# Optimization experiments

Measured on AMD Instinct MI355X. Metric: run time of the kernel, lower is better.

## Reference

```python
import jax, jax.numpy as jnp
import numpy as np

B, N, C = 8, 1024, 768
H, D = 12, 64  # num_heads, head_dim
SCALE = D ** -0.5


def setup_inputs() -> dict:
    key = jax.random.key(0)
    ks = jax.random.split(key, 6)
    x = jax.random.normal(ks[0], (B, N, C), dtype=jnp.float32)
    # per-head Linear weights stacked: [H, D, C] (torch Linear stores [out, in])
    Wq = jax.random.normal(ks[1], (H, D, C), dtype=jnp.float32) * 0.02
    Wk = jax.random.normal(ks[2], (H, D, C), dtype=jnp.float32) * 0.02
    Wv = jax.random.normal(ks[3], (H, D, C), dtype=jnp.float32) * 0.02
    Wp = jax.random.normal(ks[4], (C, C), dtype=jnp.float32) * 0.02
    bp = jnp.zeros((C,), dtype=jnp.float32)
    return {"x": x, "Wq": Wq, "Wk": Wk, "Wv": Wv, "Wp": Wp, "bp": bp}


def reference(x, Wq, Wk, Wv, Wp, bp):
    # Per-head projections (batched across heads): [B, H, N, D]
    q = jnp.einsum('bnc,hdc->bhnd', x, Wq) * SCALE
    k = jnp.einsum('bnc,hdc->bhnd', x, Wk)
    v = jnp.einsum('bnc,hdc->bhnd', x, Wv)
    # Scaled dot-product attention per head
    attn = jax.nn.softmax(jnp.einsum('bhnd,bhmd->bhnm', q, k), axis=-1)
    out = jnp.einsum('bhnm,bhmd->bhnd', attn, v)
    # Concat heads along last dim == transpose to [B, N, H, D] then reshape
    out = out.transpose(0, 2, 1, 3).reshape(x.shape[0], x.shape[1], -1)
    # Output projection
    return out @ Wp.T + bp
```

## Files before the change

### kernel.cpp

```cpp
#include <hip/hip_runtime.h>

typedef unsigned short u16;
typedef __attribute__((ext_vector_type(8))) __bf16 bf16x8;
typedef __attribute__((ext_vector_type(4))) float f32x4;
typedef __attribute__((ext_vector_type(16))) float f32x16;

__device__ __forceinline__ u16 f2bf(float f) {
    union { float f; unsigned u; } v; v.f = f;
    unsigned u = v.u;
    u += 0x7FFFu + ((u >> 16) & 1u);
    return (u16)(u >> 16);
}

__device__ __forceinline__ unsigned pk2(float lo, float hi) {
    union { __bf16 h[2]; unsigned u; } x;
    x.h[0] = (__bf16)lo; x.h[1] = (__bf16)hi;
    return x.u;
}
__device__ __forceinline__ void pswap(unsigned &a, unsigned &b) {
    auto r = __builtin_amdgcn_permlane32_swap(a, b, false, false);
    a = r[0]; b = r[1];
}

typedef const __attribute__((address_space(1))) void GV;
typedef __attribute__((address_space(3))) void LV;
__device__ __forceinline__ void gl2lds16(const void* g, void* l) {
    __builtin_amdgcn_global_load_lds((GV*)g, (LV*)l, 16, 0, 0);
}

__global__ __launch_bounds__(256) void cast_all(
    const float* __restrict__ x,  const float* __restrict__ Wq,
    const float* __restrict__ Wk, const float* __restrict__ Wv,
    const float* __restrict__ Wp,
    u16* __restrict__ xb, u16* __restrict__ wb, u16* __restrict__ wpb)
{
    int bid = blockIdx.x;
    const float4* s; ushort4* d; int idx;
    if (bid < 6144) {
        s = (const float4*)x; d = (ushort4*)xb; idx = bid * 256 + threadIdx.x;
    } else {
        int t = bid - 6144;
        int w = t / 576;
        idx = (t - w * 576) * 256 + threadIdx.x;
        s = (const float4*)(w == 0 ? Wq : w == 1 ? Wk : w == 2 ? Wv : Wp);
        d = (ushort4*)(w == 3 ? wpb : wb + w * 589824);
    }
    float4 f = s[idx];
    ushort4 o;
    o.x = f2bf(f.x); o.y = f2bf(f.y); o.z = f2bf(f.z); o.w = f2bf(f.w);
    d[idx] = o;
}

__device__ __forceinline__ void stage_c(const u16* src, int k0, u16* lds, int i) {
    int line = i >> 3, pos = i & 7;
    int p = pos ^ (line & 7);
    int r = line * 2 + (p >> 2), c = p & 3;
    gl2lds16(src + (size_t)r * 768 + k0 + c * 8, lds + i * 8);
}
__device__ __forceinline__ const bf16x8* fragK(const u16* lds, int row, int quad) {
    int line = row >> 1;
    int pos = (((row & 1) << 2) | quad) ^ (line & 7);
    return reinterpret_cast<const bf16x8*>(lds + line * 64 + pos * 8);
}

__global__ __launch_bounds__(512, 4) void gemm_qkv(
    const u16* __restrict__ A, const u16* __restrict__ Bm,
    u16* __restrict__ qo, u16* __restrict__ ko, u16* __restrict__ vto)
{
    __shared__ u16 As[3][8192];
    __shared__ u16 Bs[3][4096];
    const int tid = threadIdx.x;
    const int wave = tid >> 6, lane = tid & 63;
    const int quad = lane >> 4, l16 = lane & 15;
    const int wm = wave >> 1, wn = wave & 1;
    const int id = blockIdx.x + 18 * blockIdx.y;
    const int nid = (id & 7) * 72 + (id >> 3);
    const int bx = nid % 18, by = nid / 18;
    const int rowBase = by * 256;
    const int colBase = bx * 128;

    const u16* aSrc = A + (size_t)rowBase * 768;
    const u16* bSrc = Bm + (size_t)colBase * 768;
    f32x4 acc[4][4] = {};

    #pragma unroll
    for (int tt = 0; tt < 2; tt++) {
        stage_c(aSrc, tt * 32, As[tt], tid);
        stage_c(aSrc, tt * 32, As[tt], 512 + tid);
        stage_c(bSrc, tt * 32, Bs[tt], tid);
    }
    asm volatile("s_waitcnt vmcnt(3)" ::: "memory");
    __builtin_amdgcn_s_barrier();
    asm volatile("" ::: "memory");

    int buf = 0;
    for (int t = 0; t < 24; t++) {
        bf16x8 a[4], b[4];
        #pragma unroll
        for (int mi = 0; mi < 4; mi++) a[mi] = *fragK(As[buf], wm * 64 + mi * 16 + l16, quad);
        #pragma unroll
        for (int ni = 0; ni < 4; ni++) b[ni] = *fragK(Bs[buf], wn * 64 + ni * 16 + l16, quad);
        int sb = buf + 2; if (sb >= 3) sb -= 3;
        if (t + 2 < 24) {
            int k2 = (t + 2) * 32;
            stage_c(aSrc, k2, As[sb], tid);
            stage_c(aSrc, k2, As[sb], 512 + tid);
            stage_c(bSrc, k2, Bs[sb], tid);
        }
        if (t <= 21)      asm volatile("s_waitcnt vmcnt(3)" ::: "memory");
        else if (t == 22) asm volatile("s_waitcnt vmcnt(0)" ::: "memory");
        __builtin_amdgcn_s_barrier();
        asm volatile("" ::: "memory");
        __builtin_amdgcn_s_setprio(1);
        #pragma unroll
        for (int mi = 0; mi < 4; mi++)
            #pragma unroll
            for (int ni = 0; ni < 4; ni++)
                acc[mi][ni] = __builtin_amdgcn_mfma_f32_16x16x32_bf16(a[mi], b[ni], acc[mi][ni], 0, 0, 0);
        __builtin_amdgcn_s_setprio(0);
        buf = (buf == 2) ? 0 : buf + 1;
    }

    #pragma unroll
    for (int mi = 0; mi < 4; mi++) {
        #pragma unroll
        for (int ni = 0; ni < 4; ni++) {
            int gj = colBase + wn * 64 + ni * 16 + l16;
            int which = gj / 768;
            int r = gj - which * 768;
            int h = r >> 6, d = r & 63;
            int gi0 = rowBase + wm * 64 + mi * 16 + quad * 4;
            int b_ = gi0 >> 10;
            int n0 = gi0 & 1023;
            if (which == 2) {
                ushort4 pk;
                pk.x = f2bf(acc[mi][ni][0]);
                pk.y = f2bf(acc[mi][ni][1]);
                pk.z = f2bf(acc[mi][ni][2]);
                pk.w = f2bf(acc[mi][ni][3]);
                *reinterpret_cast<ushort4*>(vto + ((size_t)(b_ * 12 + h) * 64 + d) * 1024 + n0) = pk;
            } else {
                float s = (which == 0) ? 0.125f : 1.0f;
                u16* dst = (which == 0 ? qo : ko) + ((size_t)(b_ * 12 + h) * 1024 + n0) * 64 + d;
                #pragma unroll
                for (int rr = 0; rr < 4; rr++)
                    dst[(size_t)rr * 64] = f2bf(acc[mi][ni][rr] * s);
            }
        }
    }
}

__global__ __launch_bounds__(256, 3) void attn_fwd(
    const u16* __restrict__ q, const u16* __restrict__ k,
    const u16* __restrict__ vt, u16* __restrict__ ao)
{
    __shared__ u16 Ks[2][4096];
    __shared__ u16 Vs[2][4096];
    const int bh = blockIdx.x, qt = blockIdx.y;
    const int b = bh / 12, h = bh - b * 12;
    const int tid = threadIdx.x;
    const int wave = tid >> 6, lane = tid & 63;
    const int l31 = lane & 31, hi = lane >> 5;
    const int sw = l31 & 7;

    const u16* qb = q + (size_t)bh * 65536 + ((size_t)qt * 128 + wave * 32) * 64;
    const u16* kb = k + (size_t)bh * 65536;
    const u16* vb = vt + (size_t)bh * 65536;

    auto stage = [&](int buf, int j0) {
        #pragma unroll
        for (int r = 0; r < 2; r++) {
            int i = r * 256 + tid;
            int row = i >> 3, cp = i & 7;
            int cl = cp ^ (row & 7);
            gl2lds16((const char*)kb + (size_t)(j0 + row) * 128 + cl * 16,
                     (char*)&Ks[buf][0] + i * 16);
        }
        #pragma unroll
        for (int r = 0; r < 2; r++) {
            int i = r * 256 + tid;
            int row = i >> 3, cp = i & 7;
            int cl = cp ^ (row & 7);
            gl2lds16((const char*)vb + (size_t)row * 2048 + (size_t)j0 * 2 + cl * 16,
                     (char*)&Vs[buf][0] + i * 16);
        }
    };

    stage(0, 0);

    bf16x8 qf[4];
    #pragma unroll
    for (int dk = 0; dk < 4; dk++)
        qf[dk] = *reinterpret_cast<const bf16x8*>(qb + l31 * 64 + dk * 16 + hi * 8);

    f32x16 o0 = {}, o1 = {};
    float lsum = 0.f;

    __syncthreads();

    int buf = 0;
    for (int j0 = 0; j0 < 1024; j0 += 64) {
        if (j0 + 64 < 1024) stage(buf ^ 1, j0 + 64);

        f32x16 s0 = {}, s1 = {};
        #pragma unroll
        for (int dk = 0; dk < 4; dk++) {
            int ch = ((2 * dk + hi) ^ sw) * 8;
            bf16x8 kf0 = *reinterpret_cast<const bf16x8*>(&Ks[buf][l31 * 64 + ch]);
            bf16x8 kf1 = *reinterpret_cast<const bf16x8*>(&Ks[buf][(32 + l31) * 64 + ch]);
            s0 = __builtin_amdgcn_mfma_f32_32x32x16_bf16(kf0, qf[dk], s0, 0, 0, 0);
            s1 = __builtin_amdgcn_mfma_f32_32x32x16_bf16(kf1, qf[dk], s1, 0, 0, 0);
        }

        bf16x8 pa[4];
        #pragma unroll
        for (int kbk = 0; kbk < 2; kbk++) {
            float p[16];
            #pragma unroll
            for (int r = 0; r < 16; r++) {
                p[r] = __expf(kbk ? s1[r] : s0[r]);
                lsum += p[r];
            }
            unsigned W00 = pk2(p[0],  p[1]),  W01 = pk2(p[2],  p[3]);
            unsigned W10 = pk2(p[4],  p[5]),  W11 = pk2(p[6],  p[7]);
            unsigned W20 = pk2(p[8],  p[9]),  W21 = pk2(p[10], p[11]);
            unsigned W30 = pk2(p[12], p[13]), W31 = pk2(p[14], p[15]);
            pswap(W00, W10); pswap(W01, W11);
            pswap(W20, W30); pswap(W21, W31);
            union { unsigned u[4]; bf16x8 v; } pk0, pk1;
            pk0.u[0] = W00; pk0.u[1] = W01; pk0.u[2] = W10; pk0.u[3] = W11;
            pk1.u[0] = W20; pk1.u[1] = W21; pk1.u[2] = W30; pk1.u[3] = W31;
            pa[kbk * 2 + 0] = pk0.v;
            pa[kbk * 2 + 1] = pk1.v;
        }

        #pragma unroll
        for (int ks = 0; ks < 4; ks++) {
            int ch = ((2 * ks + hi) ^ sw) * 8;
            bf16x8 vf0 = *reinterpret_cast<const bf16x8*>(&Vs[buf][l31 * 64 + ch]);
            bf16x8 vf1 = *reinterpret_cast<const bf16x8*>(&Vs[buf][(32 + l31) * 64 + ch]);
            o0 = __builtin_amdgcn_mfma_f32_32x32x16_bf16(pa[ks], vf0, o0, 0, 0, 0);
            o1 = __builtin_amdgcn_mfma_f32_32x32x16_bf16(pa[ks], vf1, o1, 0, 0, 0);
        }

        __syncthreads();
        buf ^= 1;
    }

    lsum += __shfl_xor(lsum, 32, 64);

    #pragma unroll
    for (int r = 0; r < 16; r++) {
        int qrow = (r & 3) + 8 * (r >> 2) + 4 * hi;
        float lv = __shfl(lsum, qrow, 32);
        float inv = 1.0f / lv;
        int n = qt * 128 + wave * 32 + qrow;
        size_t base = (size_t)(b * 1024 + n) * 768 + h * 64;
        ao[base + l31]      = f2bf(o0[r] * inv);
        ao[base + 32 + l31] = f2bf(o1[r] * inv);
    }
}

__global__ __launch_bounds__(256, 3) void gemm_proj(
    const u16* __restrict__ A, const u16* __restrict__ Bm,
    const float* __restrict__ bias, float* __restrict__ out)
{
    __shared__ u16 As[3][4096];
    __shared__ u16 Bs[3][4096];
    const int tid = threadIdx.x;
    const int wave = tid >> 6, lane = tid & 63;
    const int quad = lane >> 4, l16 = lane & 15;
    const int wr = (wave >> 1) * 64, wc = (wave & 1) * 64;
    const int id = blockIdx.x + 6 * blockIdx.y;
    const int nid = (id & 7) * 48 + (id >> 3);
    const int bx = nid % 6, by = nid / 6;
    const int rowBase = by * 128;
    const int colBase = bx * 128;

    const u16* aSrc = A + (size_t)rowBase * 768;
    const u16* bSrc = Bm + (size_t)colBase * 768;
    f32x4 acc[4][4] = {};

    #pragma unroll
    for (int tt = 0; tt < 2; tt++) {
        stage_c(aSrc, tt * 32, As[tt], tid);
        stage_c(aSrc, tt * 32, As[tt], 256 + tid);
        stage_c(bSrc, tt * 32, Bs[tt], tid);
        stage_c(bSrc, tt * 32, Bs[tt], 256 + tid);
    }
    asm volatile("s_waitcnt vmcnt(4)" ::: "memory");
    __builtin_amdgcn_s_barrier();
    asm volatile("" ::: "memory");

    int buf = 0;
    for (int t = 0; t < 24; t++) {
        bf16x8 a[4], b[4];
        #pragma unroll
        for (int mi = 0; mi < 4; mi++) a[mi] = *fragK(As[buf], wr + mi * 16 + l16, quad);
        #pragma unroll
        for (int ni = 0; ni < 4; ni++) b[ni] = *fragK(Bs[buf], wc + ni * 16 + l16, quad);
        int sb = buf + 2; if (sb >= 3) sb -= 3;
        if (t + 2 < 24) {
            int k2 = (t + 2) * 32;
            stage_c(aSrc, k2, As[sb], tid);
            stage_c(aSrc, k2, As[sb], 256 + tid);
            stage_c(bSrc, k2, Bs[sb], tid);
            stage_c(bSrc, k2, Bs[sb], 256 + tid);
        }
        if (t <= 21)      asm volatile("s_waitcnt vmcnt(4)" ::: "memory");
        else if (t == 22) asm volatile("s_waitcnt vmcnt(0)" ::: "memory");
        __builtin_amdgcn_s_barrier();
        asm volatile("" ::: "memory");
        __builtin_amdgcn_s_setprio(1);
        #pragma unroll
        for (int mi = 0; mi < 4; mi++)
            #pragma unroll
            for (int ni = 0; ni < 4; ni++)
                acc[mi][ni] = __builtin_amdgcn_mfma_f32_16x16x32_bf16(a[mi], b[ni], acc[mi][ni], 0, 0, 0);
        __builtin_amdgcn_s_setprio(0);
        buf = (buf == 2) ? 0 : buf + 1;
    }

    #pragma unroll
    for (int mi = 0; mi < 4; mi++) {
        #pragma unroll
        for (int ni = 0; ni < 4; ni++) {
            int gj = colBase + wc + ni * 16 + l16;
            float bv = bias[gj];
            int gi0 = rowBase + wr + mi * 16 + quad * 4;
            #pragma unroll
            for (int rr2 = 0; rr2 < 4; rr2++)
                out[(size_t)(gi0 + rr2) * 768 + gj] = acc[mi][ni][rr2] + bv;
        }
    }
}

extern "C" void kernel_launch(void* const* d_in, const int* in_sizes, int n_in,
                              void* d_out, int out_size, void* d_ws, size_t ws_size,
                              hipStream_t stream) {
    const float* x  = (const float*)d_in[0];
    const float* Wq = (const float*)d_in[1];
    const float* Wk = (const float*)d_in[2];
    const float* Wv = (const float*)d_in[3];
    const float* Wp = (const float*)d_in[4];
    const float* bp = (const float*)d_in[5];
    float* out = (float*)d_out;

    u16* xb  = (u16*)d_ws;
    u16* wb  = xb  + 6291456;
    u16* wpb = wb  + 1769472;
    u16* qo  = wpb + 589824;
    u16* ko  = qo  + 6291456;
    u16* vto = ko  + 6291456;
    u16* ao  = vto + 6291456;

    cast_all<<<8448, 256, 0, stream>>>(x, Wq, Wk, Wv, Wp, xb, wb, wpb);
    gemm_qkv<<<dim3(18, 32), 512, 0, stream>>>(xb, wb, qo, ko, vto);
    attn_fwd<<<dim3(96, 8), 256, 0, stream>>>(qo, ko, vto, ao);
    gemm_proj<<<dim3(6, 64), 256, 0, stream>>>(ao, wpb, bp, out);
}
```

Before: 187.3 us.

## Retile QKV and projection GEMMs with smaller tiles and double buffering

Both GEMMs move from a 3-stage async pipeline with manual vmcnt waits to a simpler 2-stage double buffer synchronised by __syncthreads. QKV tiles change from 256x128 to 128x192 (576 to 768 blocks) and projection tiles from 128x128 to 128x96 (384 to 512 blocks). The aim is to fill the CUs better and raise occupancy through smaller LDS and register footprints. In exchange, per-block operand reuse drops and prefetch overlap is shallower, with a full barrier every k-step.

```diff
diff --git a/kernel.cpp b/kernel.cpp
--- a/kernel.cpp
+++ b/kernel.cpp
@@ -63,69 +63,59 @@
     return reinterpret_cast<const bf16x8*>(lds + line * 64 + pos * 8);
 }
 
-__global__ __launch_bounds__(512, 4) void gemm_qkv(
+__global__ __launch_bounds__(512, 6) void gemm_qkv(
     const u16* __restrict__ A, const u16* __restrict__ Bm,
     u16* __restrict__ qo, u16* __restrict__ ko, u16* __restrict__ vto)
 {
-    __shared__ u16 As[3][8192];
-    __shared__ u16 Bs[3][4096];
+    __shared__ u16 As[2][4096];
+    __shared__ u16 Bs[2][6144];
     const int tid = threadIdx.x;
     const int wave = tid >> 6, lane = tid & 63;
     const int quad = lane >> 4, l16 = lane & 15;
-    const int wm = wave >> 1, wn = wave & 1;
-    const int id = blockIdx.x + 18 * blockIdx.y;
-    const int nid = (id & 7) * 72 + (id >> 3);
-    const int bx = nid % 18, by = nid / 18;
-    const int rowBase = by * 256;
-    const int colBase = bx * 128;
+    const int wm = wave >> 2, wn = wave & 3;
+    const int id = blockIdx.x + 12 * blockIdx.y;
+    const int nid = (id & 7) * 96 + (id >> 3);
+    const int bx = nid % 12, by = nid / 12;
+    const int rowBase = by * 128;
+    const int colBase = bx * 192;
 
     const u16* aSrc = A + (size_t)rowBase * 768;
     const u16* bSrc = Bm + (size_t)colBase * 768;
-    f32x4 acc[4][4] = {};
-
-    #pragma unroll
-    for (int tt = 0; tt < 2; tt++) {
-        stage_c(aSrc, tt * 32, As[tt], tid);
-        stage_c(aSrc, tt * 32, As[tt], 512 + tid);
-        stage_c(bSrc, tt * 32, Bs[tt], tid);
-    }
-    asm volatile("s_waitcnt vmcnt(3)" ::: "memory");
-    __builtin_amdgcn_s_barrier();
-    asm volatile("" ::: "memory");
+    f32x4 acc[4][3] = {};
+
+    auto stage = [&](int buf, int k0) {
+        stage_c(aSrc, k0, As[buf], tid);
+        stage_c(bSrc, k0, Bs[buf], tid);
+        if (tid < 256) stage_c(bSrc, k0, Bs[buf], 512 + tid);
+    };
+
+    stage(0, 0);
+    __syncthreads();
 
     int buf = 0;
     for (int t = 0; t < 24; t++) {
-        bf16x8 a[4], b[4];
+        if (t + 1 < 24) stage(buf ^ 1, (t + 1) * 32);
+        bf16x8 a[4], b[3];
         #pragma unroll
         for (int mi = 0; mi < 4; mi++) a[mi] = *fragK(As[buf], wm * 64 + mi * 16 + l16, quad);
         #pragma unroll
-        for (int ni = 0; ni < 4; ni++) b[ni] = *fragK(Bs[buf], wn * 64 + ni * 16 + l16, quad);
-        int sb = buf + 2; if (sb >= 3) sb -= 3;
-        if (t + 2 < 24) {
-            int k2 = (t + 2) * 32;
-            stage_c(aSrc, k2, As[sb], tid);
-            stage_c(aSrc, k2, As[sb], 512 + tid);
-            stage_c(bSrc, k2, Bs[sb], tid);
-        }
-        if (t <= 21)      asm volatile("s_waitcnt vmcnt(3)" ::: "memory");
-        else if (t == 22) asm volatile("s_waitcnt vmcnt(0)" ::: "memory");
-        __builtin_amdgcn_s_barrier();
-        asm volatile("" ::: "memory");
+        for (int ni = 0; ni < 3; ni++) b[ni] = *fragK(Bs[buf], wn * 48 + ni * 16 + l16, quad);
         __builtin_amdgcn_s_setprio(1);
         #pragma unroll
         for (int mi = 0; mi < 4; mi++)
             #pragma unroll
-            for (int ni = 0; ni < 4; ni++)
+            for (int ni = 0; ni < 3; ni++)
                 acc[mi][ni] = __builtin_amdgcn_mfma_f32_16x16x32_bf16(a[mi], b[ni], acc[mi][ni], 0, 0, 0);
         __builtin_amdgcn_s_setprio(0);
-        buf = (buf == 2) ? 0 : buf + 1;
+        __syncthreads();
+        buf ^= 1;
     }
 
     #pragma unroll
     for (int mi = 0; mi < 4; mi++) {
         #pragma unroll
-        for (int ni = 0; ni < 4; ni++) {
-            int gj = colBase + wn * 64 + ni * 16 + l16;
+        for (int ni = 0; ni < 3; ni++) {
+            int gj = colBase + wn * 48 + ni * 16 + l16;
             int which = gj / 768;
             int r = gj - which * 768;
             int h = r >> 6, d = r & 63;
@@ -265,69 +255,58 @@
     const u16* __restrict__ A, const u16* __restrict__ Bm,
     const float* __restrict__ bias, float* __restrict__ out)
 {
-    __shared__ u16 As[3][4096];
-    __shared__ u16 Bs[3][4096];
+    __shared__ u16 As[2][4096];
+    __shared__ u16 Bs[2][3072];
     const int tid = threadIdx.x;
     const int wave = tid >> 6, lane = tid & 63;
     const int quad = lane >> 4, l16 = lane & 15;
-    const int wr = (wave >> 1) * 64, wc = (wave & 1) * 64;
-    const int id = blockIdx.x + 6 * blockIdx.y;
-    const int nid = (id & 7) * 48 + (id >> 3);
-    const int bx = nid % 6, by = nid / 6;
+    const int wm = wave >> 1, wn = wave & 1;
+    const int id = blockIdx.x + 8 * blockIdx.y;
+    const int nid = (id & 7) * 64 + (id >> 3);
+    const int bx = nid % 8, by = nid / 8;
     const int rowBase = by * 128;
-    const int colBase = bx * 128;
+    const int colBase = bx * 96;
 
     const u16* aSrc = A + (size_t)rowBase * 768;
     const u16* bSrc = Bm + (size_t)colBase * 768;
-    f32x4 acc[4][4] = {};
-
-    #pragma unroll
-    for (int tt = 0; tt < 2; tt++) {
-        stage_c(aSrc, tt * 32, As[tt], tid);
-        stage_c(aSrc, tt * 32, As[tt], 256 + tid);
-        stage_c(bSrc, tt * 32, Bs[tt], tid);
-        stage_c(bSrc, tt * 32, Bs[tt], 256 + tid);
-    }
-    asm volatile("s_waitcnt vmcnt(4)" ::: "memory");
-    __builtin_amdgcn_s_barrier();
-    asm volatile("" ::: "memory");
+    f32x4 acc[4][3] = {};
+
+    auto stage = [&](int buf, int k0) {
+        stage_c(aSrc, k0, As[buf], tid);
+        stage_c(aSrc, k0, As[buf], 256 + tid);
+        stage_c(bSrc, k0, Bs[buf], tid);
+        if (tid < 128) stage_c(bSrc, k0, Bs[buf], 256 + tid);
+    };
+
+    stage(0, 0);
+    __syncthreads();
 
     int buf = 0;
     for (int t = 0; t < 24; t++) {
-        bf16x8 a[4], b[4];
-        #pragma unroll
-        for (int mi = 0; mi < 4; mi++) a[mi] = *fragK(As[buf], wr + mi * 16 + l16, quad);
-        #pragma unroll
-        for (int ni = 0; ni < 4; ni++) b[ni] = *fragK(Bs[buf], wc + ni * 16 + l16, quad);
-        int sb = buf + 2; if (sb >= 3) sb -= 3;
-        if (t + 2 < 24) {
-            int k2 = (t + 2) * 32;
-            stage_c(aSrc, k2, As[sb], tid);
-            stage_c(aSrc, k2, As[sb], 256 + tid);
-            stage_c(bSrc, k2, Bs[sb], tid);
-            stage_c(bSrc, k2, Bs[sb], 256 + tid);
-        }
-        if (t <= 21)      asm volatile("s_waitcnt vmcnt(4)" ::: "memory");
-        else if (t == 22) asm volatile("s_waitcnt vmcnt(0)" ::: "memory");
-        __builtin_amdgcn_s_barrier();
-        asm volatile("" ::: "memory");
+        if (t + 1 < 24) stage(buf ^ 1, (t + 1) * 32);
+        bf16x8 a[4], b[3];
+        #pragma unroll
+        for (int mi = 0; mi < 4; mi++) a[mi] = *fragK(As[buf], wm * 64 + mi * 16 + l16, quad);
+        #pragma unroll
+        for (int ni = 0; ni < 3; ni++) b[ni] = *fragK(Bs[buf], wn * 48 + ni * 16 + l16, quad);
         __builtin_amdgcn_s_setprio(1);
         #pragma unroll
         for (int mi = 0; mi < 4; mi++)
             #pragma unroll
-            for (int ni = 0; ni < 4; ni++)
+            for (int ni = 0; ni < 3; ni++)
                 acc[mi][ni] = __builtin_amdgcn_mfma_f32_16x16x32_bf16(a[mi], b[ni], acc[mi][ni], 0, 0, 0);
         __builtin_amdgcn_s_setprio(0);
-        buf = (buf == 2) ? 0 : buf + 1;
+        __syncthreads();
+        buf ^= 1;
     }
 
     #pragma unroll
     for (int mi = 0; mi < 4; mi++) {
         #pragma unroll
-        for (int ni = 0; ni < 4; ni++) {
-            int gj = colBase + wc + ni * 16 + l16;
+        for (int ni = 0; ni < 3; ni++) {
+            int gj = colBase + wn * 48 + ni * 16 + l16;
             float bv = bias[gj];
-            int gi0 = rowBase + wr + mi * 16 + quad * 4;
+            int gi0 = rowBase + wm * 64 + mi * 16 + quad * 4;
             #pragma unroll
             for (int rr2 = 0; rr2 < 4; rr2++)
                 out[(size_t)(gi0 + rr2) * 768 + gj] = acc[mi][ni][rr2] + bv;
@@ -355,7 +334,7 @@
     u16* ao  = vto + 6291456;
 
     cast_all<<<8448, 256, 0, stream>>>(x, Wq, Wk, Wv, Wp, xb, wb, wpb);
-    gemm_qkv<<<dim3(18, 32), 512, 0, stream>>>(xb, wb, qo, ko, vto);
+    gemm_qkv<<<dim3(12, 64), 512, 0, stream>>>(xb, wb, qo, ko, vto);
     attn_fwd<<<dim3(96, 8), 256, 0, stream>>>(qo, ko, vto, ao);
-    gemm_proj<<<dim3(6, 64), 256, 0, stream>>>(ao, wpb, bp, out);
-}
+    gemm_proj<<<dim3(8, 64), 256, 0, stream>>>(ao, wpb, bp, out);
+}
```

After: 276.8 us. 1.48x slower.
